# Kernel optimization log

Measured on AMD Instinct MI355X. Metric: run time of the kernel, lower is better.

## Reference

```python
import jax, jax.numpy as jnp
import numpy as np
import math

N_HEAD = 16


def setup_inputs() -> dict:
    key = jax.random.key(0)
    ks = jax.random.split(key, 5)
    B, T, C = 2, 2048, 2048
    x = jax.random.normal(ks[0], (B, T, C), dtype=jnp.float32)
    # additive causal mask: 0 on/below diagonal, large negative above
    causal = jnp.tril(jnp.ones((T, T), dtype=bool))
    attention_mask = jnp.where(causal, 0.0, -1e9).astype(jnp.float32)[None, None]
    scale = 0.02
    W_attn = jax.random.normal(ks[1], (C, 3 * C), dtype=jnp.float32) * scale
    b_attn = jax.random.normal(ks[2], (3 * C,), dtype=jnp.float32) * scale
    W_proj = jax.random.normal(ks[3], (C, C), dtype=jnp.float32) * scale
    b_proj = jax.random.normal(ks[4], (C,), dtype=jnp.float32) * scale
    return {"x": x, "attention_mask": attention_mask, "W_attn": W_attn,
            "b_attn": b_attn, "W_proj": W_proj, "b_proj": b_proj}


def reference(x, attention_mask, W_attn, b_attn, W_proj, b_proj):
    B, T, C = x.shape
    H = N_HEAD
    Dh = C // H
    qkv = x @ W_attn + b_attn                      # [B,T,3C]
    q, k, v = jnp.split(qkv, 3, axis=2)            # each [B,T,C]
    current_cache = jnp.concatenate([k, v], axis=2)  # [B,T,2C]
    qh = q.reshape(B, T, H, Dh).transpose(0, 2, 1, 3)  # [B,H,T,Dh]
    kh = k.reshape(B, T, H, Dh).transpose(0, 2, 1, 3)
    vh = v.reshape(B, T, H, Dh).transpose(0, 2, 1, 3)
    att = jnp.einsum('bhqd,bhkd->bhqk', qh, kh) * (1.0 / math.sqrt(Dh))
    att = att + attention_mask                     # broadcast [1,1,T,T]
    att = jax.nn.softmax(att, axis=-1)
    y = jnp.einsum('bhqk,bhkd->bhqd', att, vh)     # [B,H,T,Dh]
    y = y.transpose(0, 2, 1, 3).reshape(B, T, C)
    y = y @ W_proj + b_proj                        # [B,T,C]
    return (y, current_cache)
```

## Files before the change

### kernel.cpp

```cpp
#include <hip/hip_runtime.h>

typedef __attribute__((ext_vector_type(8))) short bf16x8;
typedef __attribute__((ext_vector_type(4))) float f32x4;

#define MFMA16(a, b, c) __builtin_amdgcn_mfma_f32_16x16x32_bf16((a), (b), (c), 0, 0, 0)

static __device__ __forceinline__ short f2bf(float f) {
  unsigned u = __builtin_bit_cast(unsigned, f);
  unsigned r = (u + 0x7FFFu + ((u >> 16) & 1u)) >> 16;
  return (short)(unsigned short)r;
}
static __device__ __forceinline__ unsigned pack2(float lo, float hi) {
  return (unsigned)(unsigned short)f2bf(lo) | ((unsigned)(unsigned short)f2bf(hi) << 16);
}

static __device__ __forceinline__ void glds16(const void* g, void* l) {
  __builtin_amdgcn_global_load_lds((const __attribute__((address_space(1))) unsigned*)g,
                                   (__attribute__((address_space(3))) unsigned*)l, 16, 0, 0);
}

__global__ __launch_bounds__(256) void cvt_bf16_kernel(const float* __restrict__ in,
                                                       short* __restrict__ out) {
  size_t i = ((size_t)blockIdx.x * 256 + threadIdx.x) * 8;
  float4 a = *(const float4*)(in + i);
  float4 b = *(const float4*)(in + i + 4);
  uint4 o;
  o.x = pack2(a.x, a.y);
  o.y = pack2(a.z, a.w);
  o.z = pack2(b.x, b.y);
  o.w = pack2(b.z, b.w);
  *(uint4*)(out + i) = o;
}

__global__ __launch_bounds__(256) void transpose_cvt_kernel(const float* __restrict__ in,
                                                            short* __restrict__ out, int R,
                                                            int Cc) {
  __shared__ float tile[64][65];
  int tx = threadIdx.x & 15, ty = threadIdx.x >> 4;
  int r0 = blockIdx.y * 64, c0 = blockIdx.x * 64;
#pragma unroll
  for (int i = 0; i < 4; i++) {
    int r = ty + i * 16;
    float4 v = *(const float4*)(in + (size_t)(r0 + r) * Cc + c0 + tx * 4);
    tile[r][tx * 4 + 0] = v.x;
    tile[r][tx * 4 + 1] = v.y;
    tile[r][tx * 4 + 2] = v.z;
    tile[r][tx * 4 + 3] = v.w;
  }
  __syncthreads();
#pragma unroll
  for (int i = 0; i < 4; i++) {
    int co = ty + i * 16;
    uint2 o;
    o.x = pack2(tile[tx * 4 + 0][co], tile[tx * 4 + 1][co]);
    o.y = pack2(tile[tx * 4 + 2][co], tile[tx * 4 + 3][co]);
    *(uint2*)(out + (size_t)(c0 + co) * R + r0 + tx * 4) = o;
  }
}


#define AFQ(C, KS, MT) (*(const bf16x8*)&lds[(C)*16384 + (KS)*8192 + (wr4 + (MT)) * 512 + rdoff])
#define BFQ(C, KS, NT) \
  (*(const bf16x8*)&lds[32768 + (C)*8192 + (KS)*4096 + (wc4 + (NT)) * 512 + rdoff])

#define STAGE(C, KS, KT)                                                           \
  do {                                                                             \
    glds16(Asrc0 + (KT) * 64 + (KS) * 32, &lds[(C)*16384 + (KS)*8192 + wid * 512]); \
    glds16(Asrc1 + (KT) * 64 + (KS) * 32,                                          \
           &lds[(C)*16384 + (KS)*8192 + (wid + 8) * 512]);                         \
    glds16(Bsrc0 + (KT) * 64 + (KS) * 32,                                          \
           &lds[32768 + (C)*8192 + (KS)*4096 + wid * 512]);                        \
  } while (0)

#define MIDBAR                                                       \
  do {                                                               \
    asm volatile("s_barrier\n\ts_waitcnt lgkmcnt(0)" ::: "memory");  \
    __builtin_amdgcn_sched_barrier(0);                               \
  } while (0)
#define ENDBARV6                                                     \
  do {                                                               \
    __builtin_amdgcn_sched_barrier(0);                               \
    asm volatile("s_waitcnt vmcnt(6)\n\ts_barrier" ::: "memory");    \
    __builtin_amdgcn_sched_barrier(0);                               \
  } while (0)

#define MMROW(AR, MT)                            \
  do {                                           \
    acc[MT][0] = MFMA16(AR, bfr[0], acc[MT][0]); \
    acc[MT][1] = MFMA16(AR, bfr[1], acc[MT][1]); \
    acc[MT][2] = MFMA16(AR, bfr[2], acc[MT][2]); \
    acc[MT][3] = MFMA16(AR, bfr[3], acc[MT][3]); \
  } while (0)

#define PHASE(C, KS, STG)          \
  do {                             \
    af[0] = AFQ(C, KS, 0);         \
    af[1] = AFQ(C, KS, 1);         \
    af[2] = AFQ(C, KS, 2);         \
    af[3] = AFQ(C, KS, 3);         \
    bfr[0] = BFQ(C, KS, 0);        \
    bfr[1] = BFQ(C, KS, 1);        \
    bfr[2] = BFQ(C, KS, 2);        \
    bfr[3] = BFQ(C, KS, 3);        \
    STG;                           \
    MIDBAR;                        \
    __builtin_amdgcn_s_setprio(1); \
    MMROW(af[0], 0);               \
    MMROW(af[1], 1);               \
    MMROW(af[2], 2);               \
    MMROW(af[3], 3);               \
    __builtin_amdgcn_s_setprio(0); \
    ENDBARV6;                      \
  } while (0)

#define KTILE(C, NX, MM)                     \
  do {                                       \
    int s1 = (MM) + 1 > 31 ? 31 : (MM) + 1;  \
    int s2 = (MM) + 2 > 31 ? 31 : (MM) + 2;  \
    PHASE(C, 0, STAGE(NX, 1, s1));           \
    PHASE(C, 1, STAGE(C, 0, s2));            \
  } while (0)

#define GEMM_PREAMBLE(Aptr, Bptr)                                                  \
  __shared__ __align__(16) short lds[49152];                           \
  int tid = threadIdx.x;                                                           \
  int lane = tid & 63, wid = tid >> 6;                                             \
  int l15 = lane & 15, l4 = lane >> 4;                                             \
  int wr = wid >> 1, wc = wid & 1;                                                 \
  int wr4 = wr * 4, wc4 = wc * 4;                                                  \
  int wprime = (lane * 16) ^ (lane & 32);                                          \
  int r_ = wprime >> 6;                                                            \
  int cs_ = (wprime & 63) >> 1;                                                    \
  const short* Asrc0 = (Aptr) + (size_t)(rowBase + wid * 16 + r_) * 2048 + cs_;    \
  const short* Asrc1 = (Aptr) + (size_t)(rowBase + (wid + 8) * 16 + r_) * 2048 + cs_; \
  const short* Bsrc0 = (Bptr) + (size_t)(colBase + wid * 16 + r_) * 2048 + cs_;    \
  int rdoff = l15 * 32 + ((l4 * 8) ^ ((l15 & 8) << 1));                            \
  f32x4 zero = {0.f, 0.f, 0.f, 0.f};                                               \
  f32x4 acc[4][4];                                                                 \
  _Pragma("unroll") for (int i = 0; i < 4; i++) _Pragma("unroll") for (int j = 0;  \
                                                                       j < 4; j++) \
      acc[i][j] = zero;                                                            \
  bf16x8 af[4], bfr[4];                                                            \
  STAGE(0, 0, 0);                                                                  \
  STAGE(0, 1, 0);                                                                  \
  STAGE(1, 0, 1);                                                                  \
  asm volatile("s_waitcnt vmcnt(6)" ::: "memory");                                 \
  __builtin_amdgcn_sched_barrier(0);                                               \
  asm volatile("s_barrier" ::: "memory");                                          \
  __builtin_amdgcn_sched_barrier(0);                                               \
  for (int it = 0; it < 16; ++it) {                                                \
    int m0 = it * 2;                                                               \
    KTILE(0, 1, m0);                                                               \
    KTILE(1, 0, m0 + 1);                                                           \
  }                                                                                \
  asm volatile("s_waitcnt vmcnt(0)" ::: "memory");                                 \
  __syncthreads();

__global__ __launch_bounds__(512, 2) void gemm_qkv_kernel(const short* __restrict__ A,
                                                          const short* __restrict__ Bt,
                                                          const float* __restrict__ bias,
                                                          short* __restrict__ q_bf,
                                                          short* __restrict__ k_bf,
                                                          short* __restrict__ v_bf,
                                                          float* __restrict__ cache) {
  int bid = blockIdx.x;
  int s = (bid & 7) * 96 + (bid >> 3);
  int bx = s % 48, by = s / 48;
  int rowBase = by * 256, colBase = bx * 128;

  GEMM_PREAMBLE(A, Bt)

  int seg = colBase >> 11;
  int colLoc = colBase & 2047;
  float scale = (seg == 0) ? 0.08838834764831845f : 1.0f;
  short* outp = (seg == 0) ? q_bf : (seg == 1) ? k_bf : v_bf;
  float bv[4];
#pragma unroll
  for (int nt = 0; nt < 4; nt++) bv[nt] = bias[colBase + wc * 64 + nt * 16 + l15];

  short(*Cs)[136] = (short(*)[136])lds;
#pragma unroll
  for (int mt = 0; mt < 4; mt++)
#pragma unroll
    for (int nt = 0; nt < 4; nt++)
#pragma unroll
      for (int r = 0; r < 4; r++)
        Cs[wr * 64 + mt * 16 + l4 * 4 + r][wc * 64 + nt * 16 + l15] =
            f2bf((acc[mt][nt][r] + bv[nt]) * scale);
  __syncthreads();
#pragma unroll
  for (int pp = 0; pp < 8; pp++) {
    int idx = pp * 512 + tid;
    int row = idx >> 4, c8 = (idx & 15) * 8;
    *(uint4*)(outp + (size_t)(rowBase + row) * 2048 + colLoc + c8) = *(const uint4*)&Cs[row][c8];
  }

  if (seg) {
    int coff = (seg == 1) ? 0 : 2048;
#pragma unroll
    for (int mt = 0; mt < 4; mt++)
#pragma unroll
      for (int nt = 0; nt < 4; nt++) {
        int cc = coff + colLoc + wc * 64 + nt * 16 + l15;
#pragma unroll
        for (int r = 0; r < 4; r++) {
          int row = rowBase + wr * 64 + mt * 16 + l4 * 4 + r;
          cache[(size_t)row * 4096 + cc] = acc[mt][nt][r] + bv[nt];
        }
      }
  }
}

__global__ __launch_bounds__(512, 2) void gemm_proj_kernel(const short* __restrict__ A,
                                                           const short* __restrict__ Bt,
                                                           const float* __restrict__ bias,
                                                           float* __restrict__ out_y) {
  int bid = blockIdx.x;
  int s = (bid & 7) * 32 + (bid >> 3);
  int bx = s % 16, by = s / 16;
  int rowBase = by * 256, colBase = bx * 128;

  GEMM_PREAMBLE(A, Bt)

#pragma unroll
  for (int mt = 0; mt < 4; mt++)
#pragma unroll
    for (int nt = 0; nt < 4; nt++) {
      int col = colBase + wc * 64 + nt * 16 + l15;
      float bvv = bias[col];
#pragma unroll
      for (int r = 0; r < 4; r++) {
        int row = rowBase + wr * 64 + mt * 16 + l4 * 4 + r;
        out_y[(size_t)row * 2048 + col] = acc[mt][nt][r] + bvv;
      }
    }
}

__global__ __launch_bounds__(256) void vpost_kernel(const short* __restrict__ vb,
                                                    short* __restrict__ vt) {
  __shared__ short tile[64][72];
  int tid = threadIdx.x;
  int z = blockIdx.z;
  int b = z >> 4, hh = z & 15;
  int t0 = blockIdx.x * 64, d0 = blockIdx.y * 64;
  int tx = tid & 7, ty = tid >> 3;
#pragma unroll
  for (int i = 0; i < 2; i++) {
    int r = ty + i * 32;
    *(uint4*)&tile[r][tx * 8] =
        *(const uint4*)(vb + (size_t)(b * 2048 + t0 + r) * 2048 + hh * 128 + d0 + tx * 8);
  }
  __syncthreads();
#pragma unroll
  for (int i = 0; i < 2; i++) {
    int dr = ty + i * 32;
    short tmp[8];
#pragma unroll
    for (int j = 0; j < 8; j++) {
      int p = tx * 8 + j;
      int tl = (p & 32) + ((p & 1) << 4) + ((p >> 1) & 15);
      tmp[j] = tile[tl][dr];
    }
    *(uint4*)(vt + (size_t)(z * 128 + d0 + dr) * 2048 + t0 + tx * 8) = *(uint4*)tmp;
  }
}

#define LDK 136
#define LDV 72
#define LDP 72

__global__ __launch_bounds__(512, 4) void attn_kernel(const short* __restrict__ qb,
                                                      const short* __restrict__ kb,
                                                      const short* __restrict__ vtb,
                                                      short* __restrict__ attout) {
  __shared__ short Ks[64 * LDK];
  __shared__ short Vs[128 * LDV];
  __shared__ short Ps[8][16 * LDP];

  int tid = threadIdx.x;
  int lane = tid & 63, wid = tid >> 6;
  int l15 = lane & 15, l4 = lane >> 4;
  int qlo = blockIdx.x, qhi = 31 - qlo;
  int h = blockIdx.y, b = blockIdx.z;
  int myqt = (wid < 4) ? qhi : qlo;
  int qrow0 = myqt * 64 + (wid & 3) * 16;
  size_t qkbase = (size_t)b * 2048 * 2048 + (size_t)h * 128;
  size_t vbase = (size_t)((b * 16 + h) * 128) * 2048;

  bf16x8 qf[4];
#pragma unroll
  for (int kk = 0; kk < 4; kk++)
    qf[kk] = *(const bf16x8*)(qb + qkbase + (size_t)(qrow0 + l15) * 2048 + kk * 32 + l4 * 8);

  short onev = (short)0x3F80;
  bf16x8 ones = {onev, onev, onev, onev, onev, onev, onev, onev};

  f32x4 zero = {0.f, 0.f, 0.f, 0.f};
  f32x4 o[8], ol;
#pragma unroll
  for (int n = 0; n < 8; n++) o[n] = zero;
  ol = zero;

  for (int kt = 0; kt <= qhi; kt++) {
    int kt0 = kt * 64;
    __syncthreads();
#pragma unroll
    for (int i = 0; i < 2; i++) {
      int c = i * 512 + tid;
      int kr = c >> 4, kc = (c & 15) * 8;
      *(uint4*)&Ks[kr * LDK + kc] = *(const uint4*)(kb + qkbase + (size_t)(kt0 + kr) * 2048 + kc);
    }
#pragma unroll
    for (int i = 0; i < 2; i++) {
      int c = i * 512 + tid;
      int dr = c >> 3, tc = (c & 7) * 8;
      *(uint4*)&Vs[dr * LDV + tc] = *(const uint4*)(vtb + vbase + (size_t)dr * 2048 + kt0 + tc);
    }
    __syncthreads();

    if (wid < 4 || kt <= qlo) {
      f32x4 s[4];
#pragma unroll
      for (int nt = 0; nt < 4; nt++) s[nt] = zero;
#pragma unroll
      for (int kk = 0; kk < 4; kk++) {
#pragma unroll
        for (int nt = 0; nt < 4; nt++) {
          bf16x8 kf = *(const bf16x8*)&Ks[(nt * 16 + l15) * LDK + kk * 32 + l4 * 8];
          s[nt] = MFMA16(qf[kk], kf, s[nt]);
        }
      }

      if (kt == myqt) {
#pragma unroll
        for (int nt = 0; nt < 4; nt++) {
          int colg = kt0 + nt * 16 + l15;
#pragma unroll
          for (int r = 0; r < 4; r++) {
            int rowg = qrow0 + l4 * 4 + r;
            if (colg > rowg) s[nt][r] = -1e30f;
          }
        }
      }

#pragma unroll
      for (int r = 0; r < 4; r++) {
        float p0 = __expf(s[0][r]);
        float p1 = __expf(s[1][r]);
        float p2 = __expf(s[2][r]);
        float p3 = __expf(s[3][r]);
        int prow = (l4 * 4 + r) * LDP;
        *(unsigned*)&Ps[wid][prow + 2 * l15] = pack2(p0, p1);
        *(unsigned*)&Ps[wid][prow + 32 + 2 * l15] = pack2(p2, p3);
      }

#pragma unroll
      for (int kk = 0; kk < 2; kk++) {
        bf16x8 pf = *(const bf16x8*)&Ps[wid][l15 * LDP + kk * 32 + l4 * 8];
        ol = MFMA16(pf, ones, ol);
#pragma unroll
        for (int n = 0; n < 8; n++) {
          bf16x8 vf = *(const bf16x8*)&Vs[(n * 16 + l15) * LDV + kk * 32 + l4 * 8];
          o[n] = MFMA16(pf, vf, o[n]);
        }
      }
    }
  }

  float rl[4];
#pragma unroll
  for (int r = 0; r < 4; r++) rl[r] = 1.0f / ol[r];
#pragma unroll
  for (int n = 0; n < 8; n++)
#pragma unroll
    for (int r = 0; r < 4; r++)
      attout[qkbase + (size_t)(qrow0 + l4 * 4 + r) * 2048 + n * 16 + l15] =
          f2bf(o[n][r] * rl[r]);
}

extern "C" void kernel_launch(void* const* d_in, const int* in_sizes, int n_in, void* d_out,
                              int out_size, void* d_ws, size_t ws_size, hipStream_t stream) {
  const float* x = (const float*)d_in[0];
  const float* W_attn = (const float*)d_in[2];
  const float* b_attn = (const float*)d_in[3];
  const float* W_proj = (const float*)d_in[4];
  const float* b_proj = (const float*)d_in[5];
  float* y = (float*)d_out;
  float* cache = y + (size_t)4096 * 2048;

  char* p = (char*)d_ws;
  short* x_bf = (short*)p;   p += (size_t)8388608 * 2;
  short* q_bf = (short*)p;   p += (size_t)8388608 * 2;
  short* k_bf = (short*)p;   p += (size_t)8388608 * 2;
  short* vt_bf = (short*)p;  p += (size_t)8388608 * 2;
  short* att_bf = (short*)p; p += (size_t)8388608 * 2;
  short* wt_attn = (short*)p; p += (size_t)12582912 * 2;
  short* wt_proj = (short*)p; p += (size_t)4194304 * 2;
  short* v_bf = att_bf;

  cvt_bf16_kernel<<<4096, 256, 0, stream>>>(x, x_bf);
  transpose_cvt_kernel<<<dim3(96, 32), 256, 0, stream>>>(W_attn, wt_attn, 2048, 6144);
  transpose_cvt_kernel<<<dim3(32, 32), 256, 0, stream>>>(W_proj, wt_proj, 2048, 2048);
  gemm_qkv_kernel<<<768, 512, 0, stream>>>(x_bf, wt_attn, b_attn, q_bf, k_bf, v_bf, cache);
  vpost_kernel<<<dim3(32, 2, 32), 256, 0, stream>>>(v_bf, vt_bf);
  attn_kernel<<<dim3(16, 16, 2), 512, 0, stream>>>(q_bf, k_bf, vt_bf, att_bf);
  gemm_proj_kernel<<<256, 512, 0, stream>>>(att_bf, wt_proj, b_proj, y);
}
```

Measured before the change: 432.5 us.

## Double attention query rows per warp, prefetch K/V tiles in registers, remap GEMM blocks

```diff
diff --git a/kernel.cpp b/kernel.cpp
--- a/kernel.cpp
+++ b/kernel.cpp
@@ -164,8 +164,8 @@
                                                           short* __restrict__ v_bf,
                                                           float* __restrict__ cache) {
   int bid = blockIdx.x;
-  int s = (bid & 7) * 96 + (bid >> 3);
-  int bx = s % 48, by = s / 48;
+  int j = bid >> 3;
+  int bx = (bid & 7) * 6 + (j % 6), by = j / 6;
   int rowBase = by * 256, colBase = bx * 128;
 
   GEMM_PREAMBLE(A, Bt)
@@ -216,8 +216,8 @@
                                                            const float* __restrict__ bias,
                                                            float* __restrict__ out_y) {
   int bid = blockIdx.x;
-  int s = (bid & 7) * 32 + (bid >> 3);
-  int bx = s % 16, by = s / 16;
+  int j = bid >> 3;
+  int bx = (bid & 7) * 2 + (j & 1), by = j >> 1;
   int rowBase = by * 256, colBase = bx * 128;
 
   GEMM_PREAMBLE(A, Bt)
@@ -269,113 +269,149 @@
 #define LDV 72
 #define LDP 72
 
-__global__ __launch_bounds__(512, 4) void attn_kernel(const short* __restrict__ qb,
+__global__ __launch_bounds__(512, 2) void attn_kernel(const short* __restrict__ qb,
                                                       const short* __restrict__ kb,
                                                       const short* __restrict__ vtb,
                                                       short* __restrict__ attout) {
   __shared__ short Ks[64 * LDK];
   __shared__ short Vs[128 * LDV];
-  __shared__ short Ps[8][16 * LDP];
+  __shared__ short Ps[8][32 * LDP];
 
   int tid = threadIdx.x;
   int lane = tid & 63, wid = tid >> 6;
   int l15 = lane & 15, l4 = lane >> 4;
-  int qlo = blockIdx.x, qhi = 31 - qlo;
+  int qlo = blockIdx.x, qhi = 15 - qlo;
   int h = blockIdx.y, b = blockIdx.z;
   int myqt = (wid < 4) ? qhi : qlo;
-  int qrow0 = myqt * 64 + (wid & 3) * 16;
+  int qrow0 = myqt * 128 + (wid & 3) * 32;
+  int kdiag = qrow0 >> 6;
+  int ktmax = 2 * qhi + 1;
   size_t qkbase = (size_t)b * 2048 * 2048 + (size_t)h * 128;
   size_t vbase = (size_t)((b * 16 + h) * 128) * 2048;
 
-  bf16x8 qf[4];
-#pragma unroll
-  for (int kk = 0; kk < 4; kk++)
-    qf[kk] = *(const bf16x8*)(qb + qkbase + (size_t)(qrow0 + l15) * 2048 + kk * 32 + l4 * 8);
+  bf16x8 qf[2][4];
+#pragma unroll
+  for (int m = 0; m < 2; m++)
+#pragma unroll
+    for (int kk = 0; kk < 4; kk++)
+      qf[m][kk] =
+          *(const bf16x8*)(qb + qkbase + (size_t)(qrow0 + m * 16 + l15) * 2048 + kk * 32 + l4 * 8);
 
   short onev = (short)0x3F80;
   bf16x8 ones = {onev, onev, onev, onev, onev, onev, onev, onev};
 
   f32x4 zero = {0.f, 0.f, 0.f, 0.f};
-  f32x4 o[8], ol;
-#pragma unroll
-  for (int n = 0; n < 8; n++) o[n] = zero;
-  ol = zero;
-
-  for (int kt = 0; kt <= qhi; kt++) {
-    int kt0 = kt * 64;
+  f32x4 o[2][8], ol[2];
+#pragma unroll
+  for (int m = 0; m < 2; m++) {
+#pragma unroll
+    for (int n = 0; n < 8; n++) o[m][n] = zero;
+    ol[m] = zero;
+  }
+
+  int c0 = tid, c1 = 512 + tid;
+  int kr0 = c0 >> 4, kc0 = (c0 & 15) * 8;
+  int kr1 = c1 >> 4, kc1 = (c1 & 15) * 8;
+  int dr0 = c0 >> 3, tc0 = (c0 & 7) * 8;
+  int dr1 = c1 >> 3, tc1 = (c1 & 7) * 8;
+  const short* kA = kb + qkbase + (size_t)kr0 * 2048 + kc0;
+  const short* kB = kb + qkbase + (size_t)kr1 * 2048 + kc1;
+  const short* vA = vtb + vbase + (size_t)dr0 * 2048 + tc0;
+  const short* vB = vtb + vbase + (size_t)dr1 * 2048 + tc1;
+
+  uint4 krg0 = *(const uint4*)kA;
+  uint4 krg1 = *(const uint4*)kB;
+  uint4 vrg0 = *(const uint4*)vA;
+  uint4 vrg1 = *(const uint4*)vB;
+
+  for (int kt = 0; kt <= ktmax; kt++) {
     __syncthreads();
-#pragma unroll
-    for (int i = 0; i < 2; i++) {
-      int c = i * 512 + tid;
-      int kr = c >> 4, kc = (c & 15) * 8;
-      *(uint4*)&Ks[kr * LDK + kc] = *(const uint4*)(kb + qkbase + (size_t)(kt0 + kr) * 2048 + kc);
-    }
-#pragma unroll
-    for (int i = 0; i < 2; i++) {
-      int c = i * 512 + tid;
-      int dr = c >> 3, tc = (c & 7) * 8;
-      *(uint4*)&Vs[dr * LDV + tc] = *(const uint4*)(vtb + vbase + (size_t)dr * 2048 + kt0 + tc);
+    *(uint4*)&Ks[kr0 * LDK + kc0] = krg0;
+    *(uint4*)&Ks[kr1 * LDK + kc1] = krg1;
+    *(uint4*)&Vs[dr0 * LDV + tc0] = vrg0;
+    *(uint4*)&Vs[dr1 * LDV + tc1] = vrg1;
+    if (kt < ktmax) {
+      size_t ko = (size_t)(kt + 1) * 64 * 2048;
+      int vo = (kt + 1) * 64;
+      krg0 = *(const uint4*)(kA + ko);
+      krg1 = *(const uint4*)(kB + ko);
+      vrg0 = *(const uint4*)(vA + vo);
+      vrg1 = *(const uint4*)(vB + vo);
     }
     __syncthreads();
 
-    if (wid < 4 || kt <= qlo) {
-      f32x4 s[4];
-#pragma unroll
-      for (int nt = 0; nt < 4; nt++) s[nt] = zero;
+    if (kt <= kdiag) {
+      f32x4 s[2][4];
+#pragma unroll
+      for (int m = 0; m < 2; m++)
+#pragma unroll
+        for (int nt = 0; nt < 4; nt++) s[m][nt] = zero;
 #pragma unroll
       for (int kk = 0; kk < 4; kk++) {
 #pragma unroll
         for (int nt = 0; nt < 4; nt++) {
           bf16x8 kf = *(const bf16x8*)&Ks[(nt * 16 + l15) * LDK + kk * 32 + l4 * 8];
-          s[nt] = MFMA16(qf[kk], kf, s[nt]);
+          s[0][nt] = MFMA16(qf[0][kk], kf, s[0][nt]);
+          s[1][nt] = MFMA16(qf[1][kk], kf, s[1][nt]);
         }
       }
 
-      if (kt == myqt) {
-#pragma unroll
-        for (int nt = 0; nt < 4; nt++) {
-          int colg = kt0 + nt * 16 + l15;
-#pragma unroll
-          for (int r = 0; r < 4; r++) {
-            int rowg = qrow0 + l4 * 4 + r;
-            if (colg > rowg) s[nt][r] = -1e30f;
+      if (kt == kdiag) {
+        int kt0 = kt * 64;
+#pragma unroll
+        for (int m = 0; m < 2; m++)
+#pragma unroll
+          for (int nt = 0; nt < 4; nt++) {
+            int colg = kt0 + nt * 16 + l15;
+#pragma unroll
+            for (int r = 0; r < 4; r++) {
+              int rowg = qrow0 + m * 16 + l4 * 4 + r;
+              if (colg > rowg) s[m][nt][r] = -1e30f;
+            }
           }
+      }
+
+#pragma unroll
+      for (int m = 0; m < 2; m++)
+#pragma unroll
+        for (int r = 0; r < 4; r++) {
+          float p0 = __expf(s[m][0][r]);
+          float p1 = __expf(s[m][1][r]);
+          float p2 = __expf(s[m][2][r]);
+          float p3 = __expf(s[m][3][r]);
+          int prow = (m * 16 + l4 * 4 + r) * LDP;
+          *(unsigned*)&Ps[wid][prow + 2 * l15] = pack2(p0, p1);
+          *(unsigned*)&Ps[wid][prow + 32 + 2 * l15] = pack2(p2, p3);
         }
-      }
-
-#pragma unroll
-      for (int r = 0; r < 4; r++) {
-        float p0 = __expf(s[0][r]);
-        float p1 = __expf(s[1][r]);
-        float p2 = __expf(s[2][r]);
-        float p3 = __expf(s[3][r]);
-        int prow = (l4 * 4 + r) * LDP;
-        *(unsigned*)&Ps[wid][prow + 2 * l15] = pack2(p0, p1);
-        *(unsigned*)&Ps[wid][prow + 32 + 2 * l15] = pack2(p2, p3);
-      }
 
 #pragma unroll
       for (int kk = 0; kk < 2; kk++) {
-        bf16x8 pf = *(const bf16x8*)&Ps[wid][l15 * LDP + kk * 32 + l4 * 8];
-        ol = MFMA16(pf, ones, ol);
+        bf16x8 pf0 = *(const bf16x8*)&Ps[wid][l15 * LDP + kk * 32 + l4 * 8];
+        bf16x8 pf1 = *(const bf16x8*)&Ps[wid][(16 + l15) * LDP + kk * 32 + l4 * 8];
+        ol[0] = MFMA16(pf0, ones, ol[0]);
+        ol[1] = MFMA16(pf1, ones, ol[1]);
 #pragma unroll
         for (int n = 0; n < 8; n++) {
           bf16x8 vf = *(const bf16x8*)&Vs[(n * 16 + l15) * LDV + kk * 32 + l4 * 8];
-          o[n] = MFMA16(pf, vf, o[n]);
+          o[0][n] = MFMA16(pf0, vf, o[0][n]);
+          o[1][n] = MFMA16(pf1, vf, o[1][n]);
         }
       }
     }
   }
 
-  float rl[4];
-#pragma unroll
-  for (int r = 0; r < 4; r++) rl[r] = 1.0f / ol[r];
-#pragma unroll
-  for (int n = 0; n < 8; n++)
-#pragma unroll
-    for (int r = 0; r < 4; r++)
-      attout[qkbase + (size_t)(qrow0 + l4 * 4 + r) * 2048 + n * 16 + l15] =
-          f2bf(o[n][r] * rl[r]);
+#pragma unroll
+  for (int m = 0; m < 2; m++) {
+    float rl[4];
+#pragma unroll
+    for (int r = 0; r < 4; r++) rl[r] = 1.0f / ol[m][r];
+#pragma unroll
+    for (int n = 0; n < 8; n++)
+#pragma unroll
+      for (int r = 0; r < 4; r++)
+        attout[qkbase + (size_t)(qrow0 + m * 16 + l4 * 4 + r) * 2048 + n * 16 + l15] =
+            f2bf(o[m][n][r] * rl[r]);
+  }
 }
 
 extern "C" void kernel_launch(void* const* d_in, const int* in_sizes, int n_in, void* d_out,
@@ -403,6 +439,6 @@
   transpose_cvt_kernel<<<dim3(32, 32), 256, 0, stream>>>(W_proj, wt_proj, 2048, 2048);
   gemm_qkv_kernel<<<768, 512, 0, stream>>>(x_bf, wt_attn, b_attn, q_bf, k_bf, v_bf, cache);
   vpost_kernel<<<dim3(32, 2, 32), 256, 0, stream>>>(v_bf, vt_bf);
-  attn_kernel<<<dim3(16, 16, 2), 512, 0, stream>>>(q_bf, k_bf, vt_bf, att_bf);
+  attn_kernel<<<dim3(8, 16, 2), 512, 0, stream>>>(q_bf, k_bf, vt_bf, att_bf);
   gemm_proj_kernel<<<256, 512, 0, stream>>>(att_bf, wt_proj, b_proj, y);
 }
```

Measured after the change: 408.4 us. -5.6%, faster.
